# Performance work log

Measured on AMD Instinct MI355X. Metric: run time of the kernel, lower is better.

## Reference

```python
import jax, jax.numpy as jnp
import numpy as np

HEADS = 16
EPS = 1e-12


def setup_inputs() -> dict:
    key = jax.random.key(0)
    ks = jax.random.split(key, 5)
    B, S, H = 4, 2048, 1024
    scale = 1.0 / np.sqrt(H)
    return {
        "input": jax.random.normal(ks[0], (B, S, H), jnp.float32),
        "input_mask": jnp.zeros((B, 1, 1, S), jnp.float32),  # additive mask
        "norm_w": jnp.ones((H,), jnp.float32),
        "norm_b": jnp.zeros((H,), jnp.float32),
        "attn_qkvw": jax.random.normal(ks[1], (3 * H, H), jnp.float32) * scale,
        "attn_qkvb": jax.random.normal(ks[2], (3 * H,), jnp.float32) * 0.01,
        "attn_ow": jax.random.normal(ks[3], (H, H), jnp.float32) * scale,
    }


def reference(input, input_mask, norm_w, norm_b, attn_qkvw, attn_qkvb, attn_ow):
    B, S, H = input.shape
    d_head = H // HEADS

    # qkv_gemm: fused LayerNorm + QKV projection (pre_layer_norm path)
    mu = jnp.mean(input, axis=-1, keepdims=True)
    var = jnp.mean(jnp.square(input - mu), axis=-1, keepdims=True)
    ln = (input - mu) * jax.lax.rsqrt(var + EPS) * norm_w + norm_b
    qkv = ln @ attn_qkvw.T + attn_qkvb  # [B,S,3H]

    q, k, v = jnp.split(qkv, 3, axis=-1)  # each [B,S,H]
    key_layer, value_layer = k, v  # returned pre-transpose, as in the fused path

    qh = q.reshape(B, S, HEADS, d_head).transpose(0, 2, 1, 3)  # [B,h,S,d]
    kh = k.reshape(B, S, HEADS, d_head).transpose(0, 2, 1, 3)
    vh = v.reshape(B, S, HEADS, d_head).transpose(0, 2, 1, 3)

    # fused softmax-attention: score scale nets to 1/sqrt(d_head)
    scores = jnp.einsum("bhqd,bhkd->bhqk", qh, kh) / jnp.sqrt(
        jnp.asarray(d_head, input.dtype)) + input_mask
    p = jax.nn.softmax(scores, axis=-1)
    ctx = jnp.einsum("bhqk,bhkd->bhqd", p, vh)  # [B,h,S,d]
    context_layer = ctx.transpose(0, 2, 1, 3).reshape(B, S, H)

    # vector_matmul output projection (bias added outside this module)
    output = context_layer @ attn_ow.T
    return (output, key_layer, value_layer, context_layer)
```

## Files before the change

### kernel.cpp

```cpp
#include <hip/hip_runtime.h>
#include <cstdint>


typedef __attribute__((ext_vector_type(8))) short short8;
typedef __attribute__((ext_vector_type(4))) short short4v;
typedef __attribute__((ext_vector_type(4))) float floatx4;

#define BSH 8388608
#define PART_STRIDE 8388608
#define LOG2E 1.4426950408889634f

static __device__ __forceinline__ short f2bf(float f) {
  union { float f; uint32_t u; } v; v.f = f;
  uint32_t r = v.u + 0x7fffu + ((v.u >> 16) & 1u);
  return (short)(r >> 16);
}
static __device__ __forceinline__ short f2bf_fast(float f) {
  union { float f; uint32_t u; } v; v.f = f;
  return (short)((v.u + 0x8000u) >> 16);
}

typedef __attribute__((address_space(1))) void gas_t;
typedef __attribute__((address_space(3))) void las_t;
static __device__ __forceinline__ void async16(const void* g, const void* l) {
  __builtin_amdgcn_global_load_lds((gas_t*)(uintptr_t)g,
                                   (las_t*)(uint32_t)(uintptr_t)l, 16, 0, 0);
}

__global__ __launch_bounds__(256) void k_convert(const float4* __restrict__ wqkv,
                                                 const float4* __restrict__ ow,
                                                 short4v* __restrict__ dq,
                                                 short4v* __restrict__ dow) {
  const int n1 = (3072 * 1024) / 4, n2 = (1024 * 1024) / 4;
  for (int i = blockIdx.x * 256 + threadIdx.x; i < n1 + n2; i += gridDim.x * 256) {
    float4 v = (i < n1) ? wqkv[i] : ow[i - n1];
    short4v s;
    s[0] = f2bf(v.x); s[1] = f2bf(v.y); s[2] = f2bf(v.z); s[3] = f2bf(v.w);
    if (i < n1) dq[i] = s; else dow[i - n1] = s;
  }
}

__global__ __launch_bounds__(256) void k_ln(const float* __restrict__ x,
                                            const float* __restrict__ w,
                                            const float* __restrict__ bb,
                                            short* __restrict__ out) {
  const int row = blockIdx.x, t = threadIdx.x;
  float4 v = ((const float4*)(x + row * 1024))[t];
  float s = v.x + v.y + v.z + v.w;
  float sq = v.x * v.x + v.y * v.y + v.z * v.z + v.w * v.w;
#pragma unroll
  for (int off = 32; off; off >>= 1) { s += __shfl_down(s, off); sq += __shfl_down(sq, off); }
  __shared__ float ls[4], lq[4];
  if ((t & 63) == 0) { ls[t >> 6] = s; lq[t >> 6] = sq; }
  __syncthreads();
  s = ls[0] + ls[1] + ls[2] + ls[3];
  sq = lq[0] + lq[1] + lq[2] + lq[3];
  float mu = s * (1.0f / 1024.0f);
  float var = sq * (1.0f / 1024.0f) - mu * mu;
  float rs = rsqrtf(fmaxf(var, 0.0f) + 1e-12f);
  float4 wv = ((const float4*)w)[t];
  float4 bv = ((const float4*)bb)[t];
  short4v o;
  o[0] = f2bf((v.x - mu) * rs * wv.x + bv.x);
  o[1] = f2bf((v.y - mu) * rs * wv.y + bv.y);
  o[2] = f2bf((v.z - mu) * rs * wv.z + bv.z);
  o[3] = f2bf((v.w - mu) * rs * wv.w + bv.w);
  ((short4v*)out)[row * 256 + t] = o;
}

template <int MODE>
__global__ __launch_bounds__(256) void k_gemm(const short* __restrict__ A,
                                              const short* __restrict__ Bm,
                                              const float* __restrict__ bias,
                                              float* __restrict__ out,
                                              short* __restrict__ qkvh,
                                              int K, int N) {
  __shared__ short As[128 * 32], Bs[128 * 32];
  const int tid = threadIdx.x, lane = tid & 63, w = tid >> 6;
  const int quad = lane >> 4, l15 = lane & 15;
  const int wr = w >> 1, wc = w & 1;
  const int m0 = blockIdx.y * 128, n0 = blockIdx.x * 128;
  floatx4 acc[4][4] = {};
  for (int k0 = 0; k0 < K; k0 += 32) {
    __syncthreads();
#pragma unroll
    for (int r = 0; r < 2; r++) {
      int pb = r * 256 + w * 64;
      int p = pb + lane;
      int row = p >> 2, c = (p & 3) ^ ((p >> 3) & 3);
      async16(&A[(m0 + row) * K + k0 + c * 8], &As[pb * 8]);
      async16(&Bm[(n0 + row) * K + k0 + c * 8], &Bs[pb * 8]);
    }
    __syncthreads();
    short8 af[4], bf[4];
#pragma unroll
    for (int i = 0; i < 4; i++) {
      int ar = wr * 64 + i * 16 + l15;
      af[i] = *(const short8*)&As[ar * 32 + ((quad ^ ((ar >> 1) & 3)) * 8)];
      int br = wc * 64 + i * 16 + l15;
      bf[i] = *(const short8*)&Bs[br * 32 + ((quad ^ ((br >> 1) & 3)) * 8)];
    }
#pragma unroll
    for (int i = 0; i < 4; i++)
#pragma unroll
      for (int j = 0; j < 4; j++)
        acc[i][j] = __builtin_amdgcn_mfma_f32_16x16x32_bf16(af[i], bf[j], acc[i][j], 0, 0, 0);
  }
  const int grB = m0 + wr * 64, gcB = n0 + wc * 64;
  const float QS = 0.125f * LOG2E;
#pragma unroll
  for (int i = 0; i < 4; i++) {
#pragma unroll
    for (int j = 0; j < 4; j++) {
      int gc = gcB + j * 16 + l15;
      if (MODE == 0) {
        float bv = bias[gc];
        int part = gc >> 10, within = gc & 1023;
        int head = within >> 6, dd = within & 63;
#pragma unroll
        for (int reg = 0; reg < 4; reg++) {
          int gr = grB + i * 16 + quad * 4 + reg;
          float val = acc[i][j][reg] + bv;
          int b_ = gr >> 11, s_ = gr & 2047;
          int hs = (b_ * 16 + head);
          if (part == 0) {
            qkvh[(hs * 2048 + s_) * 64 + dd] = f2bf(val * QS);
          } else if (part == 1) {
            qkvh[PART_STRIDE + (hs * 2048 + s_) * 64 + dd] = f2bf(val);
            out[BSH + gr * 1024 + within] = val;
          } else {
            out[2 * BSH + gr * 1024 + within] = val;
          }
        }
      } else {
#pragma unroll
        for (int reg = 0; reg < 4; reg++) {
          int gr = grB + i * 16 + quad * 4 + reg;
          out[gr * N + gc] = acc[i][j][reg];
        }
      }
    }
  }
}

__global__ __launch_bounds__(256) void k_vt(const float* __restrict__ vsrc,
                                            short* __restrict__ vt) {
  const int st = blockIdx.x, h = blockIdx.y, b = blockIdx.z;
  const int t = threadIdx.x;
  __shared__ short Ls[64 * 64];
  const int s0 = st * 64;
#pragma unroll
  for (int j = 0; j < 4; j++) {
    int flat = j * 1024 + t * 4;
    int sl = flat >> 6, d = flat & 63;
    float4 v4 = *(const float4*)&vsrc[(size_t)(b * 2048 + s0 + sl) * 1024 + h * 64 + d];
    short4v s4;
    s4[0] = f2bf(v4.x); s4[1] = f2bf(v4.y); s4[2] = f2bf(v4.z); s4[3] = f2bf(v4.w);
    *(short4v*)&Ls[sl * 64 + (((d >> 3) ^ (sl & 7)) * 8) + (d & 7)] = s4;
  }
  __syncthreads();
  const int d = t >> 2, sbase = (t & 3) * 16;
#pragma unroll
  for (int half = 0; half < 2; half++) {
    short8 o;
#pragma unroll
    for (int j = 0; j < 8; j++) {
      int s = sbase + half * 8 + j;
      o[j] = Ls[s * 64 + (((d >> 3) ^ (s & 7)) * 8) + (d & 7)];
    }
    *(short8*)&vt[(size_t)((b * 16 + h) * 64 + d) * 2048 + s0 + sbase + half * 8] = o;
  }
}

__global__ __launch_bounds__(256, 4) void k_attn(const short* __restrict__ qkvh,
                                                 const float* __restrict__ mask,
                                                 float* __restrict__ ctx_out,
                                                 short* __restrict__ ctx_bf) {
  const int qt = blockIdx.x, h = blockIdx.y, b = blockIdx.z;
  const int tid = threadIdx.x, lane = tid & 63, w = tid >> 6;
  const int quad = lane >> 4, l15 = lane & 15;
  __shared__ short Ks[2][64 * 64];
  __shared__ short Vt[2][64 * 64];
  __shared__ short Pl[64 * 64];
  const short* qg = qkvh + (size_t)(b * 16 + h) * 2048 * 64;
  const short* kg = qg + PART_STRIDE;
  const short* vg = qkvh + 2 * PART_STRIDE + (size_t)(b * 16 + h) * 64 * 2048;
  const float* mb = mask + b * 2048;

  short8 qf[2];
  const int qr = qt * 64 + w * 16 + l15;
#pragma unroll
  for (int ks = 0; ks < 2; ks++)
    qf[ks] = *(const short8*)&qg[qr * 64 + ks * 32 + quad * 8];

  short8 ones;
#pragma unroll
  for (int j = 0; j < 8; j++) ones[j] = (short)0x3F80;

  floatx4 accO[4] = {};
  floatx4 accL = {};

  auto stage = [&](int kt, int bi) {
#pragma unroll
    for (int r = 0; r < 2; r++) {
      int pb = r * 256 + w * 64;
      int p = pb + lane;
      int row = p >> 3, c = (p & 7) ^ (row & 7);
      async16(&kg[(kt * 64 + row) * 64 + c * 8], &Ks[bi][pb * 8]);
      async16(&vg[row * 2048 + kt * 64 + c * 8], &Vt[bi][pb * 8]);
    }
  };
  stage(0, 0);

  for (int kt = 0; kt < 32; kt++) {
    const int cur = kt & 1;
    __syncthreads();
    if (kt + 1 < 32) stage(kt + 1, cur ^ 1);

    float mv[4];
#pragma unroll
    for (int nt = 0; nt < 4; nt++) mv[nt] = mb[kt * 64 + nt * 16 + l15] * LOG2E;

    floatx4 sc[4] = {};
#pragma unroll
    for (int nt = 0; nt < 4; nt++) {
      int krow = nt * 16 + l15;
#pragma unroll
      for (int ks = 0; ks < 2; ks++) {
        short8 kf = *(const short8*)&Ks[cur][krow * 64 + (((ks * 4 + quad) ^ (krow & 7)) * 8)];
        sc[nt] = __builtin_amdgcn_mfma_f32_16x16x32_bf16(qf[ks], kf, sc[nt], 0, 0, 0);
      }
    }

#pragma unroll
    for (int nt = 0; nt < 4; nt++) {
      int colc = nt * 2 + (l15 >> 3);
#pragma unroll
      for (int reg = 0; reg < 4; reg++) {
        float p = __builtin_amdgcn_exp2f(sc[nt][reg] + mv[nt]);
        int prow = w * 16 + quad * 4 + reg;
        Pl[prow * 64 + ((colc ^ (prow & 7)) * 8) + (l15 & 7)] = f2bf_fast(p);
      }
    }

#pragma unroll
    for (int ks2 = 0; ks2 < 2; ks2++) {
      int prow = w * 16 + l15;
      short8 pf = *(const short8*)&Pl[prow * 64 + (((ks2 * 4 + quad) ^ (prow & 7)) * 8)];
      accL = __builtin_amdgcn_mfma_f32_16x16x32_bf16(pf, ones, accL, 0, 0, 0);
#pragma unroll
      for (int nt2 = 0; nt2 < 4; nt2++) {
        int vrow = nt2 * 16 + l15;
        short8 vf = *(const short8*)&Vt[cur][vrow * 64 + (((ks2 * 4 + quad) ^ (vrow & 7)) * 8)];
        accO[nt2] = __builtin_amdgcn_mfma_f32_16x16x32_bf16(pf, vf, accO[nt2], 0, 0, 0);
      }
    }
  }

  float inv[4];
#pragma unroll
  for (int reg = 0; reg < 4; reg++) inv[reg] = 1.0f / accL[reg];
#pragma unroll
  for (int nt2 = 0; nt2 < 4; nt2++)
#pragma unroll
    for (int reg = 0; reg < 4; reg++) {
      int qrow = qt * 64 + w * 16 + quad * 4 + reg;
      int col = h * 64 + nt2 * 16 + l15;
      int gi = (b * 2048 + qrow) * 1024 + col;
      float val = accO[nt2][reg] * inv[reg];
      ctx_out[gi] = val;
      ctx_bf[gi] = f2bf(val);
    }
}

extern "C" void kernel_launch(void* const* d_in, const int* in_sizes, int n_in,
                              void* d_out, int out_size, void* d_ws, size_t ws_size,
                              hipStream_t stream) {
  const float* x    = (const float*)d_in[0];
  const float* mask = (const float*)d_in[1];
  const float* nw   = (const float*)d_in[2];
  const float* nb   = (const float*)d_in[3];
  const float* wqkv = (const float*)d_in[4];
  const float* bqkv = (const float*)d_in[5];
  const float* ow   = (const float*)d_in[6];
  float* out = (float*)d_out;
  char* ws = (char*)d_ws;

  short* lnb   = (short*)ws;
  short* wqkvb = (short*)(ws + 16777216);
  short* owb   = (short*)(ws + 23068672);
  short* qkvh  = (short*)(ws + 25165824);
  short* vt    = qkvh + 2 * (size_t)PART_STRIDE;

  k_convert<<<512, 256, 0, stream>>>((const float4*)wqkv, (const float4*)ow,
                                     (short4v*)wqkvb, (short4v*)owb);
  k_ln<<<8192, 256, 0, stream>>>(x, nw, nb, lnb);
  k_gemm<0><<<dim3(24, 64), 256, 0, stream>>>(lnb, wqkvb, bqkv, out, qkvh, 1024, 3072);
  k_vt<<<dim3(32, 16, 4), 256, 0, stream>>>(out + 2 * (size_t)BSH, vt);
  k_attn<<<dim3(32, 16, 4), 256, 0, stream>>>(qkvh, mask, out + 3 * (size_t)BSH, lnb);
  k_gemm<1><<<dim3(8, 64), 256, 0, stream>>>(lnb, owb, nullptr, out, nullptr, 1024, 1024);
}
```

Baseline: 418.4 us.

## Process 128 query rows per attention block to reuse staged K/V tiles

The attention kernel now gives each wave two 16-row query tiles (128 rows per block), so each K/V tile staged into LDS feeds twice as many MFMAs, and the grid is halved. The QK^T MFMA swaps operands so scores come out transposed, which lets P be written to per-wave LDS as 4-element vector stores and the mask be loaded as float4. This adds register pressure (launch bounds lowered to 3 blocks per CU) and halves the number of blocks, which may reduce occupancy.

```diff
diff --git a/kernel.cpp b/kernel.cpp
--- a/kernel.cpp
+++ b/kernel.cpp
@@ -172,7 +172,7 @@
   }
 }
 
-__global__ __launch_bounds__(256, 4) void k_attn(const short* __restrict__ qkvh,
+__global__ __launch_bounds__(256, 3) void k_attn(const short* __restrict__ qkvh,
                                                  const float* __restrict__ mask,
                                                  float* __restrict__ ctx_out,
                                                  short* __restrict__ ctx_bf) {
@@ -181,24 +181,27 @@
   const int quad = lane >> 4, l15 = lane & 15;
   __shared__ short Ks[2][64 * 64];
   __shared__ short Vt[2][64 * 64];
-  __shared__ short Pl[64 * 64];
+  __shared__ short Pl[4][32 * 64];
   const short* qg = qkvh + (size_t)(b * 16 + h) * 2048 * 64;
   const short* kg = qg + PART_STRIDE;
   const short* vg = qkvh + 2 * PART_STRIDE + (size_t)(b * 16 + h) * 64 * 2048;
   const float* mb = mask + b * 2048;
 
-  short8 qf[2];
-  const int qr = qt * 64 + w * 16 + l15;
-#pragma unroll
-  for (int ks = 0; ks < 2; ks++)
-    qf[ks] = *(const short8*)&qg[qr * 64 + ks * 32 + quad * 8];
+  short8 qf[2][2];
+#pragma unroll
+  for (int rt = 0; rt < 2; rt++) {
+    const int qr = qt * 128 + w * 32 + rt * 16 + l15;
+#pragma unroll
+    for (int ks = 0; ks < 2; ks++)
+      qf[rt][ks] = *(const short8*)&qg[qr * 64 + ks * 32 + quad * 8];
+  }
 
   short8 ones;
 #pragma unroll
   for (int j = 0; j < 8; j++) ones[j] = (short)0x3F80;
 
-  floatx4 accO[4] = {};
-  floatx4 accL = {};
+  floatx4 accO[2][4] = {};
+  floatx4 accL[2] = {};
 
   auto stage = [&](int kt, int bi) {
 #pragma unroll
@@ -217,60 +220,78 @@
     __syncthreads();
     if (kt + 1 < 32) stage(kt + 1, cur ^ 1);
 
-    float mv[4];
-#pragma unroll
-    for (int nt = 0; nt < 4; nt++) mv[nt] = mb[kt * 64 + nt * 16 + l15] * LOG2E;
-
-    floatx4 sc[4] = {};
+    float mv[4][4];
 #pragma unroll
     for (int nt = 0; nt < 4; nt++) {
-      int krow = nt * 16 + l15;
+      float4 t = *(const float4*)&mb[kt * 64 + nt * 16 + quad * 4];
+      mv[nt][0] = t.x; mv[nt][1] = t.y; mv[nt][2] = t.z; mv[nt][3] = t.w;
+    }
+
+    floatx4 sc[2][4] = {};
+#pragma unroll
+    for (int nt = 0; nt < 4; nt++) {
+      const int krow = nt * 16 + l15;
 #pragma unroll
       for (int ks = 0; ks < 2; ks++) {
         short8 kf = *(const short8*)&Ks[cur][krow * 64 + (((ks * 4 + quad) ^ (krow & 7)) * 8)];
-        sc[nt] = __builtin_amdgcn_mfma_f32_16x16x32_bf16(qf[ks], kf, sc[nt], 0, 0, 0);
-      }
-    }
-
-#pragma unroll
-    for (int nt = 0; nt < 4; nt++) {
-      int colc = nt * 2 + (l15 >> 3);
+        sc[0][nt] = __builtin_amdgcn_mfma_f32_16x16x32_bf16(kf, qf[0][ks], sc[0][nt], 0, 0, 0);
+        sc[1][nt] = __builtin_amdgcn_mfma_f32_16x16x32_bf16(kf, qf[1][ks], sc[1][nt], 0, 0, 0);
+      }
+    }
+
+#pragma unroll
+    for (int rt = 0; rt < 2; rt++) {
+      const int qb = rt * 16 + l15;
+      const int base = qb * 64 + (quad & 1) * 4;
+      const int sw = qb & 7;
+#pragma unroll
+      for (int nt = 0; nt < 4; nt++) {
+        const int v = nt * 2 + (quad >> 1);
+        short4v p4;
+#pragma unroll
+        for (int reg = 0; reg < 4; reg++)
+          p4[reg] = f2bf_fast(__builtin_amdgcn_exp2f(
+              fmaf(mv[nt][reg], LOG2E, sc[rt][nt][reg])));
+        *(short4v*)&Pl[w][base + ((v ^ sw) * 8)] = p4;
+      }
+    }
+
+#pragma unroll
+    for (int ks2 = 0; ks2 < 2; ks2++) {
+      short8 pf[2];
+#pragma unroll
+      for (int rt = 0; rt < 2; rt++) {
+        const int prow = rt * 16 + l15;
+        pf[rt] = *(const short8*)&Pl[w][prow * 64 + (((ks2 * 4 + quad) ^ (prow & 7)) * 8)];
+        accL[rt] = __builtin_amdgcn_mfma_f32_16x16x32_bf16(pf[rt], ones, accL[rt], 0, 0, 0);
+      }
+#pragma unroll
+      for (int nt2 = 0; nt2 < 4; nt2++) {
+        const int vrow = nt2 * 16 + l15;
+        short8 vf = *(const short8*)&Vt[cur][vrow * 64 + (((ks2 * 4 + quad) ^ (vrow & 7)) * 8)];
+        accO[0][nt2] = __builtin_amdgcn_mfma_f32_16x16x32_bf16(pf[0], vf, accO[0][nt2], 0, 0, 0);
+        accO[1][nt2] = __builtin_amdgcn_mfma_f32_16x16x32_bf16(pf[1], vf, accO[1][nt2], 0, 0, 0);
+      }
+    }
+  }
+
+#pragma unroll
+  for (int rt = 0; rt < 2; rt++) {
+    float inv[4];
+#pragma unroll
+    for (int reg = 0; reg < 4; reg++) inv[reg] = 1.0f / accL[rt][reg];
+#pragma unroll
+    for (int nt2 = 0; nt2 < 4; nt2++)
 #pragma unroll
       for (int reg = 0; reg < 4; reg++) {
-        float p = __builtin_amdgcn_exp2f(sc[nt][reg] + mv[nt]);
-        int prow = w * 16 + quad * 4 + reg;
-        Pl[prow * 64 + ((colc ^ (prow & 7)) * 8) + (l15 & 7)] = f2bf_fast(p);
-      }
-    }
-
-#pragma unroll
-    for (int ks2 = 0; ks2 < 2; ks2++) {
-      int prow = w * 16 + l15;
-      short8 pf = *(const short8*)&Pl[prow * 64 + (((ks2 * 4 + quad) ^ (prow & 7)) * 8)];
-      accL = __builtin_amdgcn_mfma_f32_16x16x32_bf16(pf, ones, accL, 0, 0, 0);
-#pragma unroll
-      for (int nt2 = 0; nt2 < 4; nt2++) {
-        int vrow = nt2 * 16 + l15;
-        short8 vf = *(const short8*)&Vt[cur][vrow * 64 + (((ks2 * 4 + quad) ^ (vrow & 7)) * 8)];
-        accO[nt2] = __builtin_amdgcn_mfma_f32_16x16x32_bf16(pf, vf, accO[nt2], 0, 0, 0);
-      }
-    }
-  }
-
-  float inv[4];
-#pragma unroll
-  for (int reg = 0; reg < 4; reg++) inv[reg] = 1.0f / accL[reg];
-#pragma unroll
-  for (int nt2 = 0; nt2 < 4; nt2++)
-#pragma unroll
-    for (int reg = 0; reg < 4; reg++) {
-      int qrow = qt * 64 + w * 16 + quad * 4 + reg;
-      int col = h * 64 + nt2 * 16 + l15;
-      int gi = (b * 2048 + qrow) * 1024 + col;
-      float val = accO[nt2][reg] * inv[reg];
-      ctx_out[gi] = val;
-      ctx_bf[gi] = f2bf(val);
-    }
+        const int qrow = qt * 128 + w * 32 + rt * 16 + quad * 4 + reg;
+        const int col = h * 64 + nt2 * 16 + l15;
+        const int gi = (b * 2048 + qrow) * 1024 + col;
+        float val = accO[rt][nt2][reg] * inv[reg];
+        ctx_out[gi] = val;
+        ctx_bf[gi] = f2bf(val);
+      }
+  }
 }
 
 extern "C" void kernel_launch(void* const* d_in, const int* in_sizes, int n_in,
@@ -297,6 +318,6 @@
   k_ln<<<8192, 256, 0, stream>>>(x, nw, nb, lnb);
   k_gemm<0><<<dim3(24, 64), 256, 0, stream>>>(lnb, wqkvb, bqkv, out, qkvh, 1024, 3072);
   k_vt<<<dim3(32, 16, 4), 256, 0, stream>>>(out + 2 * (size_t)BSH, vt);
-  k_attn<<<dim3(32, 16, 4), 256, 0, stream>>>(qkvh, mask, out + 3 * (size_t)BSH, lnb);
+  k_attn<<<dim3(16, 16, 4), 256, 0, stream>>>(qkvh, mask, out + 3 * (size_t)BSH, lnb);
   k_gemm<1><<<dim3(8, 64), 256, 0, stream>>>(lnb, owb, nullptr, out, nullptr, 1024, 1024);
 }
```

Measured after the change: 405.8 us. 3.0% less time.
